# Optimization experiments

Hardware: AMD Instinct MI355X
Metric: run time of the kernel (lower is better)

Reference implementation:

```python
import jax, jax.numpy as jnp
import numpy as np

D = 1024
H = 8
DK = D // H
DFF = 4 * D
EPS = 1e-6


def layer_norm(x, g, b):
    mu = jnp.mean(x, axis=-1, keepdims=True)
    var = jnp.mean(jnp.square(x - mu), axis=-1, keepdims=True)
    return (x - mu) * jax.lax.rsqrt(var + EPS) * g + b


def setup_inputs() -> dict:
    key = jax.random.key(0)
    ks = jax.random.split(key, 8)
    s = 0.02
    return {
        "x": jax.random.normal(ks[0], (4, 2048, D), dtype=jnp.float32),
        "Wq": jax.random.normal(ks[1], (D, D), dtype=jnp.float32) * s,
        "bq": jnp.zeros((D,), dtype=jnp.float32),
        "Wk": jax.random.normal(ks[2], (D, D), dtype=jnp.float32) * s,
        "bk": jnp.zeros((D,), dtype=jnp.float32),
        "Wv": jax.random.normal(ks[3], (D, D), dtype=jnp.float32) * s,
        "bv": jnp.zeros((D,), dtype=jnp.float32),
        "ln1_g": jnp.ones((D,), dtype=jnp.float32),
        "ln1_b": jnp.zeros((D,), dtype=jnp.float32),
        "W1": jax.random.normal(ks[4], (D, DFF), dtype=jnp.float32) * s,
        "b1": jnp.zeros((DFF,), dtype=jnp.float32),
        "W2": jax.random.normal(ks[5], (DFF, D), dtype=jnp.float32) * s,
        "b2": jnp.zeros((D,), dtype=jnp.float32),
        "ln2_g": jnp.ones((D,), dtype=jnp.float32),
        "ln2_b": jnp.zeros((D,), dtype=jnp.float32),
    }


def reference(x, Wq, bq, Wk, bk, Wv, bv, ln1_g, ln1_b, W1, b1, W2, b2, ln2_g, ln2_b):
    B, S, _ = x.shape

    def split_heads(t):  # [B,S,D] -> [B,H,S,dk]
        return t.reshape(B, S, H, DK).transpose(0, 2, 1, 3)

    Q = split_heads(x @ Wq + bq)
    K = split_heads(x @ Wk + bk)
    V = split_heads(x @ Wv + bv)

    scores = jnp.einsum("bhqd,bhkd->bhqk", Q, K) / jnp.sqrt(jnp.float32(DK))
    attn = jax.nn.softmax(scores, axis=-1)  # dropout is identity at eval
    out = jnp.einsum("bhqk,bhkd->bhqd", attn, V)
    out = out.transpose(0, 2, 1, 3).reshape(B, S, D)
    x1 = layer_norm(out + x, ln1_g, ln1_b)

    h = jax.nn.relu(x1 @ W1 + b1) @ W2 + b2  # dropout identity at eval
    return layer_norm(h + x1, ln2_g, ln2_b)
```

## Files before the change

kernel.cpp:

```cpp
#include <hip/hip_runtime.h>
#include <hip/hip_bf16.h>
#include <stdint.h>

#define D_MODEL 1024
#define NHEADS  8
#define DKH     128
#define DFF     4096
#define SEQ     2048
#define BATCH   4
#define NTOK    (BATCH*SEQ)
#define QKS     2048
#define QSCALE  0.12751743f

typedef float  f32x4  __attribute__((ext_vector_type(4)));
typedef __bf16 bf16x8 __attribute__((ext_vector_type(8)));

static __device__ __forceinline__ float b2f(ushort u) {
    union { uint32_t i; float f; } v; v.i = ((uint32_t)u) << 16; return v.f;
}
static __device__ __forceinline__ ushort f2b(float f) {
    union { float f; uint32_t i; } v; v.f = f;
    uint32_t r = v.i + 0x7fffu + ((v.i >> 16) & 1u);
    return (ushort)(r >> 16);
}
static __device__ __forceinline__ ushort f2b_native(float f) {
    __bf16 h = (__bf16)f;
    return __builtin_bit_cast(ushort, h);
}
static __device__ __forceinline__ float exp2_hw(float x) {
    return __builtin_amdgcn_exp2f(x);
}
static __device__ __forceinline__ void gl_lds16(const void* g, void* l) {
    __builtin_amdgcn_global_load_lds(
        (const __attribute__((address_space(1))) void*)g,
        (__attribute__((address_space(3))) void*)l, 16, 0, 0);
}
static __device__ __forceinline__ float dpp_max16(float x) {
    int t;
    t = __builtin_amdgcn_update_dpp(0, __builtin_bit_cast(int, x), 0xB1, 0xF, 0xF, true);
    x = fmaxf(x, __builtin_bit_cast(float, t));
    t = __builtin_amdgcn_update_dpp(0, __builtin_bit_cast(int, x), 0x4E, 0xF, 0xF, true);
    x = fmaxf(x, __builtin_bit_cast(float, t));
    t = __builtin_amdgcn_update_dpp(0, __builtin_bit_cast(int, x), 0x141, 0xF, 0xF, true);
    x = fmaxf(x, __builtin_bit_cast(float, t));
    t = __builtin_amdgcn_update_dpp(0, __builtin_bit_cast(int, x), 0x140, 0xF, 0xF, true);
    x = fmaxf(x, __builtin_bit_cast(float, t));
    return x;
}

__global__ __launch_bounds__(256) void conv_kernel(
    const float* __restrict__ in, ushort* __restrict__ out, int n)
{
    for (int i = (blockIdx.x * 256 + threadIdx.x) * 4; i < n; i += gridDim.x * 1024) {
        float4 v = *(const float4*)(in + i);
        ushort o[4] = { f2b(v.x), f2b(v.y), f2b(v.z), f2b(v.w) };
        *(uint2*)(out + i) = *(const uint2*)o;
    }
}

__global__ __launch_bounds__(256) void tconv_kernel(
    const float* __restrict__ in, ushort* __restrict__ out, int R, int C)
{
    __shared__ float L[32][33];
    const int tid = threadIdx.x;
    const int tx = tid & 31, ty = tid >> 5;
    const int nbc = C >> 5;
    const int r0 = (blockIdx.x / nbc) << 5;
    const int c0 = (blockIdx.x % nbc) << 5;
    #pragma unroll
    for (int p = 0; p < 4; ++p)
        L[ty + 8 * p][tx] = in[(size_t)(r0 + ty + 8 * p) * C + c0 + tx];
    __syncthreads();
    #pragma unroll
    for (int p = 0; p < 4; ++p)
        out[(size_t)(c0 + ty + 8 * p) * R + r0 + tx] = f2b(L[tx][ty + 8 * p]);
}

__global__ __launch_bounds__(256) void cat3_kernel(
    const float* __restrict__ a, const float* __restrict__ b,
    const float* __restrict__ c, float* __restrict__ out)
{
    const int i = blockIdx.x * 256 + threadIdx.x;
    out[i] = (i < 1024) ? a[i] : (i < 2048) ? b[i - 1024] : c[i - 2048];
}

__global__ __launch_bounds__(512, 2) void gemm8_relu(
    const ushort* __restrict__ A, const ushort* __restrict__ Bt,
    const float* __restrict__ bias, ushort* __restrict__ C,
    int M, int N, int K)
{
    __shared__ __align__(16) ushort lds[65536];

    const int tid  = threadIdx.x;
    const int w    = tid >> 6;
    const int lane = tid & 63;
    const int l16  = lane & 15;
    const int quad = (lane >> 4) & 3;
    const int wm   = w >> 2;
    const int wn   = w & 3;

    const int nbn = N >> 8;
    const int m0  = (blockIdx.x / nbn) << 8;
    const int n0  = (blockIdx.x % nbn) << 8;

    const int rsub = tid >> 3;
    const int gsw  = (tid & 7) ^ (rsub & 7);
    const ushort* Asrc = A  + (size_t)(m0 + rsub) * K + gsw * 8;
    const ushort* Bsrc = Bt + (size_t)(n0 + rsub) * K + gsw * 8;

    auto issue_half = [&](int p, int kt, int d) {
        const ushort* src;
        int base;
        if (p < 2) { src = Asrc + (size_t)(p * 128) * K;       base = d * 16384 + p * 8192; }
        else       { src = Bsrc + (size_t)((p - 2) * 128) * K; base = 32768 + d * 16384 + (p - 2) * 8192; }
        src += kt * 64;
        gl_lds16(src,                  &lds[base + w * 512]);
        gl_lds16(src + (size_t)64 * K, &lds[base + w * 512 + 4096]);
    };

    f32x4  acc[8][4] = {};
    bf16x8 bfr[4];

    auto phase = [&](int cur, int ks, int mq, bool readB) {
        const int Ab = cur * 16384 + wm * 8192;
        const int Bb = 32768 + cur * 16384 + (wn >> 1) * 8192;
        if (readB) {
            #pragma unroll
            for (int nt = 0; nt < 4; ++nt) {
                const int rB = ((wn & 1) << 6) + nt * 16 + l16;
                const int gB = ((ks << 2) + quad) ^ (rB & 7);
                bfr[nt] = *(const bf16x8*)&lds[Bb + rB * 64 + gB * 8];
            }
        }
        bf16x8 afr[4];
        #pragma unroll
        for (int mt = 0; mt < 4; ++mt) {
            const int rA = mq * 64 + mt * 16 + l16;
            const int gA = ((ks << 2) + quad) ^ (rA & 7);
            afr[mt] = *(const bf16x8*)&lds[Ab + rA * 64 + gA * 8];
        }
        __builtin_amdgcn_s_setprio(1);
        #pragma unroll
        for (int mt = 0; mt < 4; ++mt)
            #pragma unroll
            for (int nt = 0; nt < 4; ++nt)
                acc[mq * 4 + mt][nt] = __builtin_amdgcn_mfma_f32_16x16x32_bf16(
                    afr[mt], bfr[nt], acc[mq * 4 + mt][nt], 0, 0, 0);
        __builtin_amdgcn_s_setprio(0);
    };

    const int NT = K >> 6;

    #pragma unroll
    for (int p = 0; p < 4; ++p) issue_half(p, 0, 0);
    issue_half(0, 1, 1);
    asm volatile("s_waitcnt vmcnt(2)" ::: "memory");
    __builtin_amdgcn_sched_barrier(0);
    __builtin_amdgcn_s_barrier();
    __builtin_amdgcn_sched_barrier(0);

    for (int t = 0; t < NT; ++t) {
        const int  cur = t & 1;
        const bool pf  = (t + 1 < NT);

        if (pf) issue_half(1, t + 1, cur ^ 1);
        phase(cur, 0, 0, true);
        if (pf) issue_half(2, t + 1, cur ^ 1);
        phase(cur, 0, 1, false);
        if (pf) issue_half(3, t + 1, cur ^ 1);
        phase(cur, 1, 0, true);
        phase(cur, 1, 1, false);

        __builtin_amdgcn_sched_barrier(0);
        __builtin_amdgcn_s_barrier();
        __builtin_amdgcn_sched_barrier(0);
        if (pf) {
            if (t + 2 < NT) {
                issue_half(0, t + 2, cur);
                asm volatile("s_waitcnt vmcnt(2)" ::: "memory");
            } else {
                asm volatile("s_waitcnt vmcnt(0)" ::: "memory");
            }
            __builtin_amdgcn_sched_barrier(0);
            __builtin_amdgcn_s_barrier();
            __builtin_amdgcn_sched_barrier(0);
        }
    }
    __builtin_amdgcn_sched_barrier(0);

    #pragma unroll
    for (int nt = 0; nt < 4; ++nt) {
        const int n = n0 + wn * 64 + nt * 16 + l16;
        const float bv = bias[n];
        #pragma unroll
        for (int a = 0; a < 8; ++a) {
            const int mrow = m0 + wm * 128 + (a >> 2) * 64 + (a & 3) * 16 + (quad << 2);
            #pragma unroll
            for (int r = 0; r < 4; ++r) {
                const float v = fmaxf(acc[a][nt][r] + bv, 0.f);
                C[(size_t)(mrow + r) * N + n] = f2b(v);
            }
        }
    }
}

template<int MODE>
__global__ __launch_bounds__(512, 2) void gemm12(
    const ushort* __restrict__ A, const ushort* __restrict__ Bt,
    const float* __restrict__ bias, ushort* __restrict__ C,
    ushort* __restrict__ C2, int M, int N, int K)
{
    __shared__ __align__(16) ushort lds[49152];

    const int tid  = threadIdx.x;
    const int w    = tid >> 6;
    const int lane = tid & 63;
    const int l16  = lane & 15;
    const int quad = (lane >> 4) & 3;
    const int wm   = w >> 2;
    const int wn   = w & 3;

    const int cpx  = gridDim.x >> 3;
    const int bidx = (blockIdx.x & 7) * cpx + (blockIdx.x >> 3);

    int tix = bidx, kbeg = 0, kend = K, sl = 0;
    if (MODE == 3) {
        const int tiles = (M >> 7) * (N >> 8);
        sl   = bidx / tiles;
        tix  = bidx % tiles;
        kbeg = sl * (K >> 1);
        kend = kbeg + (K >> 1);
    }
    const int nbn = N >> 8;
    const int m0  = (tix / nbn) << 7;
    const int n0  = (tix % nbn) << 8;

    const int rsub = tid >> 3;
    const int gsw  = (tid & 7) ^ (rsub & 7);
    const ushort* Asrc = A  + (size_t)(m0 + rsub) * K + gsw * 8 + kbeg;
    const ushort* Bsrc = Bt + (size_t)(n0 + rsub) * K + gsw * 8 + kbeg;

    auto issue_half = [&](int p, int kt, int d) {
        const ushort* src;
        int base;
        if (p == 0) { src = Asrc;                              base = d * 8192; }
        else        { src = Bsrc + (size_t)((p - 1) * 128) * K; base = 16384 + d * 16384 + (p - 1) * 8192; }
        src += kt * 64;
        gl_lds16(src,                  &lds[base + w * 512]);
        gl_lds16(src + (size_t)64 * K, &lds[base + w * 512 + 4096]);
    };

    f32x4 acc[4][4] = {};

    auto phase = [&](int cur, int ks) {
        const int Ab = cur * 8192;
        const int Bb = 16384 + cur * 16384;
        bf16x8 afr[4], bfr[4];
        #pragma unroll
        for (int nt = 0; nt < 4; ++nt) {
            const int rB = wn * 64 + nt * 16 + l16;
            const int gB = ((ks << 2) + quad) ^ (rB & 7);
            bfr[nt] = *(const bf16x8*)&lds[Bb + rB * 64 + gB * 8];
        }
        #pragma unroll
        for (int mt = 0; mt < 4; ++mt) {
            const int rA = wm * 64 + mt * 16 + l16;
            const int gA = ((ks << 2) + quad) ^ (rA & 7);
            afr[mt] = *(const bf16x8*)&lds[Ab + rA * 64 + gA * 8];
        }
        __builtin_amdgcn_s_setprio(1);
        #pragma unroll
        for (int mt = 0; mt < 4; ++mt)
            #pragma unroll
            for (int nt = 0; nt < 4; ++nt)
                acc[mt][nt] = __builtin_amdgcn_mfma_f32_16x16x32_bf16(
                    afr[mt], bfr[nt], acc[mt][nt], 0, 0, 0);
        __builtin_amdgcn_s_setprio(0);
    };

    const int NT = (kend - kbeg) >> 6;

    issue_half(0, 0, 0);
    issue_half(1, 0, 0);
    issue_half(2, 0, 0);
    issue_half(0, 1, 1);
    asm volatile("s_waitcnt vmcnt(2)" ::: "memory");
    __builtin_amdgcn_sched_barrier(0);
    __builtin_amdgcn_s_barrier();
    __builtin_amdgcn_sched_barrier(0);

    for (int t = 0; t < NT; ++t) {
        const int  cur = t & 1;
        const bool pf  = (t + 1 < NT);

        if (pf) issue_half(1, t + 1, cur ^ 1);
        phase(cur, 0);
        if (pf) issue_half(2, t + 1, cur ^ 1);
        phase(cur, 1);

        __builtin_amdgcn_sched_barrier(0);
        __builtin_amdgcn_s_barrier();
        __builtin_amdgcn_sched_barrier(0);
        if (pf) {
            if (t + 2 < NT) {
                issue_half(0, t + 2, cur);
                asm volatile("s_waitcnt vmcnt(2)" ::: "memory");
            } else {
                asm volatile("s_waitcnt vmcnt(0)" ::: "memory");
            }
            __builtin_amdgcn_sched_barrier(0);
            __builtin_amdgcn_s_barrier();
            __builtin_amdgcn_sched_barrier(0);
        }
    }
    __builtin_amdgcn_sched_barrier(0);

    if (MODE == 2 && n0 >= 2048) {
        #pragma unroll
        for (int nt = 0; nt < 4; ++nt) {
            const int n  = n0 + wn * 64 + nt * 16 + l16;
            const int hd = n - 2048;
            const float bv = bias[n];
            const size_t vrow = (size_t)(hd >> 7) * 128 + (hd & 127);
            #pragma unroll
            for (int mt = 0; mt < 4; ++mt) {
                const int m = m0 + wm * 64 + mt * 16 + (quad << 2);
                const size_t row = (size_t)(m >> 11) * 1024 + vrow;
                ushort pk[4];
                #pragma unroll
                for (int r = 0; r < 4; ++r) pk[r] = f2b(acc[mt][nt][r] + bv);
                *(uint2*)(C2 + row * SEQ + (m & 2047)) = *(const uint2*)pk;
            }
        }
    } else if (MODE == 2) {
        const float qs = (n0 < 1024) ? QSCALE : 1.f;
        #pragma unroll
        for (int nt = 0; nt < 4; ++nt) {
            const int n = n0 + wn * 64 + nt * 16 + l16;
            const float bv = bias[n];
            #pragma unroll
            for (int mt = 0; mt < 4; ++mt) {
                #pragma unroll
                for (int r = 0; r < 4; ++r) {
                    const int m = m0 + wm * 64 + mt * 16 + (quad << 2) + r;
                    C[(size_t)m * QKS + n] = f2b((acc[mt][nt][r] + bv) * qs);
                }
            }
        }
    } else {
        ushort* Co = sl ? C2 : C;
        #pragma unroll
        for (int nt = 0; nt < 4; ++nt) {
            const int n = n0 + wn * 64 + nt * 16 + l16;
            const float bv = sl ? 0.f : bias[n];
            #pragma unroll
            for (int mt = 0; mt < 4; ++mt) {
                #pragma unroll
                for (int r = 0; r < 4; ++r) {
                    const int m = m0 + wm * 64 + mt * 16 + (quad << 2) + r;
                    Co[(size_t)m * N + n] = f2b(acc[mt][nt][r] + bv);
                }
            }
        }
    }
}

__global__ __launch_bounds__(256) void attn_kernel(
    ushort* __restrict__ qk, const ushort* __restrict__ vt)
{
    __shared__ __align__(16) ushort smem[40960];
    ushort* Ks = smem;
    ushort* Vs = smem + 16384;
    ushort* Ps = smem + 32768;

    const int tid  = threadIdx.x;
    const int w    = tid >> 6;
    const int lane = tid & 63;
    const int l16  = lane & 15;
    const int quad = lane >> 4;

    const int bid = ((blockIdx.x & 7) << 7) + (blockIdx.x >> 3);
    const int qb  = bid & 31;
    const int h   = (bid >> 5) & 7;
    const int b   = bid >> 8;

    ushort* Qp = qk + ((size_t)(b * SEQ + qb * 64)) * QKS + h * DKH;
    const ushort* Kp = qk + ((size_t)(b * SEQ)) * QKS + 1024 + h * DKH;
    const ushort* Vp = vt + ((size_t)((b * 8 + h) * 128)) * SEQ;

    #pragma unroll
    for (int i = 0; i < 4; ++i) {
        const int row = w * 16 + i * 4 + quad;
        const int g = (l16 & 8) | ((l16 & 7) ^ (row & 7));
        gl_lds16(Qp + (size_t)row * QKS + g * 8, Vs + (w * 16 + i * 4) * 128);
    }
    #pragma unroll
    for (int i = 0; i < 8; ++i) {
        const int row = w * 32 + i * 4 + quad;
        const int g = (l16 & 8) | ((l16 & 7) ^ (row & 7));
        gl_lds16(Kp + (size_t)row * QKS + g * 8, Ks + (w * 32 + i * 4) * 128);
    }
    __syncthreads();

    bf16x8 aq[4];
    {
        const int r = w * 16 + l16;
        #pragma unroll
        for (int kq = 0; kq < 4; ++kq) {
            const int gk = kq * 4 + quad;
            const int g = (gk & 8) | ((gk & 7) ^ (r & 7));
            aq[kq] = *(const bf16x8*)&Vs[r * 128 + g * 8];
        }
    }
    __syncthreads();

    #pragma unroll
    for (int i = 0; i < 8; ++i) {
        const int d = w * 32 + i * 4 + quad;
        const int g = (l16 & 8) | ((l16 & 7) ^ (d & 7));
        gl_lds16(Vp + (size_t)d * SEQ + g * 8, Vs + (w * 32 + i * 4) * 128);
    }

    f32x4 o[8] = {};
    float mrun[4], lrun[4];
    #pragma unroll
    for (int r = 0; r < 4; ++r) { mrun[r] = -1e30f; lrun[r] = 0.f; }

    for (int t = 0; t < SEQ / 128; ++t) {
        f32x4 s[8] = {};
        #pragma unroll
        for (int nt = 0; nt < 8; ++nt) {
            const int rk = nt * 16 + l16;
            #pragma unroll
            for (int kq = 0; kq < 4; ++kq) {
                const int gk = kq * 4 + quad;
                const int g = (gk & 8) | ((gk & 7) ^ (rk & 7));
                bf16x8 bk = *(const bf16x8*)&Ks[rk * 128 + g * 8];
                s[nt] = __builtin_amdgcn_mfma_f32_16x16x32_bf16(aq[kq], bk, s[nt], 0, 0, 0);
            }
        }
        __syncthreads();

        if (t + 1 < SEQ / 128) {
            #pragma unroll
            for (int i = 0; i < 8; ++i) {
                const int row = w * 32 + i * 4 + quad;
                const int g = (l16 & 8) | ((l16 & 7) ^ (row & 7));
                gl_lds16(Kp + ((size_t)((t + 1) * 128 + row)) * QKS + g * 8,
                         Ks + (w * 32 + i * 4) * 128);
            }
        }

        float vmax[4];
        #pragma unroll
        for (int r = 0; r < 4; ++r) {
            float v = s[0][r];
            #pragma unroll
            for (int nt = 1; nt < 8; ++nt) v = fmaxf(v, s[nt][r]);
            vmax[r] = dpp_max16(v);
        }
        const int grew = (vmax[0] > mrun[0]) | (vmax[1] > mrun[1]) |
                         (vmax[2] > mrun[2]) | (vmax[3] > mrun[3]);
        if (__any(grew)) {
            #pragma unroll
            for (int r = 0; r < 4; ++r) {
                const float mnew = fmaxf(mrun[r], vmax[r]);
                const float alpha = exp2_hw(mrun[r] - mnew);
                mrun[r] = mnew;
                lrun[r] *= alpha;
                #pragma unroll
                for (int nt8 = 0; nt8 < 8; ++nt8)
                    o[nt8][r] *= alpha;
            }
        }
        #pragma unroll
        for (int nt = 0; nt < 8; ++nt)
            #pragma unroll
            for (int r = 0; r < 4; ++r) {
                const float p = exp2_hw(s[nt][r] - mrun[r]);
                lrun[r] += p;
                const int row = w * 16 + (quad << 2) + r;
                Ps[row * 128 + ((nt * 16 + l16) ^ ((row & 15) << 3))] = f2b_native(p);
            }

        #pragma unroll
        for (int kp = 0; kp < 4; ++kp) {
            const int rowp = w * 16 + l16;
            const int gp = kp * 4 + quad;
            const int gsw2 = gp ^ (rowp & 15);
            bf16x8 ap = *(const bf16x8*)&Ps[rowp * 128 + gsw2 * 8];
            #pragma unroll
            for (int nt8 = 0; nt8 < 8; ++nt8) {
                const int d = nt8 * 16 + l16;
                const int gv = (gp & 8) | ((gp & 7) ^ (d & 7));
                bf16x8 bv = *(const bf16x8*)&Vs[d * 128 + gv * 8];
                o[nt8] = __builtin_amdgcn_mfma_f32_16x16x32_bf16(ap, bv, o[nt8], 0, 0, 0);
            }
        }
        __syncthreads();

        if (t + 1 < SEQ / 128) {
            #pragma unroll
            for (int i = 0; i < 8; ++i) {
                const int d = w * 32 + i * 4 + quad;
                const int g = (l16 & 8) | ((l16 & 7) ^ (d & 7));
                gl_lds16(Vp + (size_t)d * SEQ + (t + 1) * 128 + g * 8,
                         Vs + (w * 32 + i * 4) * 128);
            }
        }
    }

    #pragma unroll
    for (int r = 0; r < 4; ++r) {
        float v = lrun[r];
        #pragma unroll
        for (int msk = 1; msk <= 8; msk <<= 1)
            v += __shfl_xor(v, msk, 64);
        lrun[r] = v;
    }
    #pragma unroll
    for (int r = 0; r < 4; ++r) {
        const float inv = 1.f / lrun[r];
        const int row = w * 16 + (quad << 2) + r;
        #pragma unroll
        for (int nt8 = 0; nt8 < 8; ++nt8)
            Qp[(size_t)row * QKS + nt8 * 16 + l16] = f2b_native(o[nt8][r] * inv);
    }
}

__global__ __launch_bounds__(256) void ln_kernel(
    const ushort* __restrict__ a, int astride, const ushort* __restrict__ a2,
    const void* __restrict__ res, int res_f32,
    const float* __restrict__ g, const float* __restrict__ be,
    void* __restrict__ out, int out_f32)
{
    __shared__ float red[8];
    const int row = blockIdx.x;
    const int tid = threadIdx.x;
    const int col = tid * 4;

    ushort av[4];
    *(uint2*)av = *(const uint2*)(a + (size_t)row * astride + col);

    float v[4];
    if (res_f32) {
        float4 rr = *(const float4*)((const float*)res + (size_t)row * D_MODEL + col);
        v[0] = b2f(av[0]) + rr.x; v[1] = b2f(av[1]) + rr.y;
        v[2] = b2f(av[2]) + rr.z; v[3] = b2f(av[3]) + rr.w;
    } else {
        ushort rv[4];
        *(uint2*)rv = *(const uint2*)((const ushort*)res + (size_t)row * D_MODEL + col);
        #pragma unroll
        for (int i = 0; i < 4; ++i) v[i] = b2f(av[i]) + b2f(rv[i]);
    }
    if (a2) {
        ushort bv[4];
        *(uint2*)bv = *(const uint2*)(a2 + (size_t)row * D_MODEL + col);
        #pragma unroll
        for (int i = 0; i < 4; ++i) v[i] += b2f(bv[i]);
    }

    float s = v[0] + v[1] + v[2] + v[3];
    #pragma unroll
    for (int m = 1; m <= 32; m <<= 1) s += __shfl_xor(s, m, 64);
    if ((tid & 63) == 0) red[tid >> 6] = s;
    __syncthreads();
    const float mu = (red[0] + red[1] + red[2] + red[3]) * (1.f / D_MODEL);

    float q = 0.f;
    #pragma unroll
    for (int i = 0; i < 4; ++i) { const float d = v[i] - mu; q += d * d; }
    #pragma unroll
    for (int m = 1; m <= 32; m <<= 1) q += __shfl_xor(q, m, 64);
    if ((tid & 63) == 0) red[4 + (tid >> 6)] = q;
    __syncthreads();
    const float var = (red[4] + red[5] + red[6] + red[7]) * (1.f / D_MODEL);
    const float rstd = rsqrtf(var + 1e-6f);

    float4 gg = *(const float4*)(g + col);
    float4 bb = *(const float4*)(be + col);
    float y[4];
    y[0] = (v[0] - mu) * rstd * gg.x + bb.x;
    y[1] = (v[1] - mu) * rstd * gg.y + bb.y;
    y[2] = (v[2] - mu) * rstd * gg.z + bb.z;
    y[3] = (v[3] - mu) * rstd * gg.w + bb.w;

    if (out_f32) {
        float4 ov; ov.x = y[0]; ov.y = y[1]; ov.z = y[2]; ov.w = y[3];
        *(float4*)((float*)out + (size_t)row * D_MODEL + col) = ov;
    } else {
        ushort ov[4] = { f2b(y[0]), f2b(y[1]), f2b(y[2]), f2b(y[3]) };
        *(uint2*)((ushort*)out + (size_t)row * D_MODEL + col) = *(const uint2*)ov;
    }
}

__global__ __launch_bounds__(256) void sentinel_kernel(float* out, float S, int n) {
    for (int i = blockIdx.x * 256 + threadIdx.x; i < n; i += gridDim.x * 256)
        out[i] = S;
}

extern "C" void kernel_launch(void* const* d_in, const int* in_sizes, int n_in,
                              void* d_out, int out_size, void* d_ws, size_t ws_size,
                              hipStream_t stream)
{
    const float* x   = (const float*)d_in[0];
    const float* Wq  = (const float*)d_in[1];
    const float* bq  = (const float*)d_in[2];
    const float* Wk  = (const float*)d_in[3];
    const float* bk  = (const float*)d_in[4];
    const float* Wv  = (const float*)d_in[5];
    const float* bv  = (const float*)d_in[6];
    const float* g1  = (const float*)d_in[7];
    const float* be1 = (const float*)d_in[8];
    const float* W1  = (const float*)d_in[9];
    const float* b1  = (const float*)d_in[10];
    const float* W2  = (const float*)d_in[11];
    const float* b2  = (const float*)d_in[12];
    const float* g2  = (const float*)d_in[13];
    const float* be2 = (const float*)d_in[14];

    const size_t MB = 1024 * 1024;
    dim3 blk(256);

    if (ws_size < 88 * MB) {
        int k = (int)(ws_size >> 23); if (k > 127) k = 127;
        sentinel_kernel<<<dim3(2048), blk, 0, stream>>>(
            (float*)d_out, 1024.f + 8.f * (float)k, out_size);
        return;
    }

    char* ws = (char*)d_ws;
    ushort* qkb    = (ushort*)(ws);
    ushort* vtb    = (ushort*)(ws + 32 * MB);
    ushort* ffn0   = (ushort*)(ws);
    ushort* ffn1   = (ushort*)(ws + 16 * MB);
    ushort* xb     = (ushort*)(ws + 48 * MB);
    ushort* x1     = (ushort*)(ws + 48 * MB);
    ushort* wqkv_t = (ushort*)(ws + 64 * MB);
    ushort* w1t    = (ushort*)(ws + 70 * MB);
    ushort* w2t    = (ushort*)(ws + 78 * MB);
    float*  bqkv   = (float*) (ws + 86 * MB);
    ushort* hbuf   = (ushort*)d_out;

    conv_kernel<<<dim3(2048), blk, 0, stream>>>(x, xb, NTOK * D_MODEL);
    tconv_kernel<<<dim3(1024), blk, 0, stream>>>(Wq, wqkv_t,               1024, 1024);
    tconv_kernel<<<dim3(1024), blk, 0, stream>>>(Wk, wqkv_t + 1024 * 1024, 1024, 1024);
    tconv_kernel<<<dim3(1024), blk, 0, stream>>>(Wv, wqkv_t + 2048 * 1024, 1024, 1024);
    tconv_kernel<<<dim3(4096), blk, 0, stream>>>(W1, w1t, 1024, 4096);
    tconv_kernel<<<dim3(4096), blk, 0, stream>>>(W2, w2t, 4096, 1024);
    cat3_kernel<<<dim3(12), blk, 0, stream>>>(bq, bk, bv, bqkv);

    gemm12<2><<<dim3(64 * 12), dim3(512), 0, stream>>>(
        xb, wqkv_t, bqkv, qkb, vtb, NTOK, 3072, D_MODEL);

    attn_kernel<<<dim3(BATCH * NHEADS * (SEQ / 64)), blk, 0, stream>>>(qkb, vtb);

    ln_kernel<<<dim3(NTOK), blk, 0, stream>>>(qkb, QKS, nullptr, x, 1, g1, be1, x1, 0);

    for (int c = 0; c < 2; ++c) {
        const size_t ro = (size_t)c * 4096;
        gemm8_relu<<<dim3(16 * 16), dim3(512), 0, stream>>>(
            x1 + ro * D_MODEL, w1t, b1, hbuf, 4096, DFF, D_MODEL);
        gemm12<3><<<dim3(2 * 32 * 4), dim3(512), 0, stream>>>(
            hbuf, w2t, b2, ffn0 + ro * D_MODEL, ffn1 + ro * D_MODEL,
            4096, D_MODEL, DFF);
    }

    ln_kernel<<<dim3(NTOK), blk, 0, stream>>>(ffn0, D_MODEL, ffn1, x1, 0,
                                              g2, be2, d_out, 1);
}
```

Measured before the change: 511.3 us.

## Process 128 query rows per attention block with interleaved softmax and MFMA

The attention kernel now handles two 64-row query sub-tiles per block, so each K/V tile loaded into LDS is reused twice and global K/V traffic per query is halved. The two sub-tiles are software-pipelined: the softmax of one sub-tile is placed between the MFMA phases of the other, and s_setprio raises wave priority around the MFMA sections to encourage overlap. The three Q/K/V weight transpose launches are merged into a single kernel. In exchange, register pressure roughly doubles for accumulators and the grid is halved, which may lower occupancy and wave count.

Measured after the change: 582.3 us. 13.9% more time.

```diff
diff --git a/kernel.cpp b/kernel.cpp
--- a/kernel.cpp
+++ b/kernel.cpp
@@ -76,6 +76,28 @@
         out[(size_t)(c0 + ty + 8 * p) * R + r0 + tx] = f2b(L[tx][ty + 8 * p]);
 }
 
+__global__ __launch_bounds__(256) void tconv3_kernel(
+    const float* __restrict__ a, const float* __restrict__ b,
+    const float* __restrict__ c, ushort* __restrict__ out)
+{
+    __shared__ float L[32][33];
+    const int which = blockIdx.x >> 10;
+    const float* in = (which == 0) ? a : (which == 1) ? b : c;
+    ushort* o = out + (size_t)which * 1024 * 1024;
+    const int bix = blockIdx.x & 1023;
+    const int tid = threadIdx.x;
+    const int tx = tid & 31, ty = tid >> 5;
+    const int r0 = (bix >> 5) << 5;
+    const int c0 = (bix & 31) << 5;
+    #pragma unroll
+    for (int p = 0; p < 4; ++p)
+        L[ty + 8 * p][tx] = in[(size_t)(r0 + ty + 8 * p) * 1024 + c0 + tx];
+    __syncthreads();
+    #pragma unroll
+    for (int p = 0; p < 4; ++p)
+        o[(size_t)(c0 + ty + 8 * p) * 1024 + r0 + tx] = f2b(L[tx][ty + 8 * p]);
+}
+
 __global__ __launch_bounds__(256) void cat3_kernel(
     const float* __restrict__ a, const float* __restrict__ b,
     const float* __restrict__ c, float* __restrict__ out)
@@ -379,37 +401,33 @@
     const int l16  = lane & 15;
     const int quad = lane >> 4;
 
-    const int bid = ((blockIdx.x & 7) << 7) + (blockIdx.x >> 3);
-    const int qb  = bid & 31;
-    const int h   = (bid >> 5) & 7;
-    const int b   = bid >> 8;
-
-    ushort* Qp = qk + ((size_t)(b * SEQ + qb * 64)) * QKS + h * DKH;
+    const int bid = ((blockIdx.x & 7) << 6) + (blockIdx.x >> 3);
+    const int qb  = bid & 15;
+    const int h   = (bid >> 4) & 7;
+    const int b   = bid >> 7;
+
+    ushort* Qp = qk + ((size_t)(b * SEQ + qb * 128)) * QKS + h * DKH;
     const ushort* Kp = qk + ((size_t)(b * SEQ)) * QKS + 1024 + h * DKH;
     const ushort* Vp = vt + ((size_t)((b * 8 + h) * 128)) * SEQ;
 
-    #pragma unroll
-    for (int i = 0; i < 4; ++i) {
-        const int row = w * 16 + i * 4 + quad;
-        const int g = (l16 & 8) | ((l16 & 7) ^ (row & 7));
-        gl_lds16(Qp + (size_t)row * QKS + g * 8, Vs + (w * 16 + i * 4) * 128);
-    }
     #pragma unroll
     for (int i = 0; i < 8; ++i) {
         const int row = w * 32 + i * 4 + quad;
         const int g = (l16 & 8) | ((l16 & 7) ^ (row & 7));
+        gl_lds16(Qp + (size_t)row * QKS + g * 8, Vs + (w * 32 + i * 4) * 128);
         gl_lds16(Kp + (size_t)row * QKS + g * 8, Ks + (w * 32 + i * 4) * 128);
     }
     __syncthreads();
 
-    bf16x8 aq[4];
-    {
-        const int r = w * 16 + l16;
+    bf16x8 aq[2][4];
+    #pragma unroll
+    for (int st = 0; st < 2; ++st) {
+        const int r = st * 64 + w * 16 + l16;
         #pragma unroll
         for (int kq = 0; kq < 4; ++kq) {
             const int gk = kq * 4 + quad;
             const int g = (gk & 8) | ((gk & 7) ^ (r & 7));
-            aq[kq] = *(const bf16x8*)&Vs[r * 128 + g * 8];
+            aq[st][kq] = *(const bf16x8*)&Vs[r * 128 + g * 8];
         }
     }
     __syncthreads();
@@ -421,13 +439,19 @@
         gl_lds16(Vp + (size_t)d * SEQ + g * 8, Vs + (w * 32 + i * 4) * 128);
     }
 
-    f32x4 o[8] = {};
-    float mrun[4], lrun[4];
-    #pragma unroll
-    for (int r = 0; r < 4; ++r) { mrun[r] = -1e30f; lrun[r] = 0.f; }
+    f32x4 o[2][8] = {};
+    float mrun[2][4], lrun[2][4];
+    #pragma unroll
+    for (int st = 0; st < 2; ++st)
+        #pragma unroll
+        for (int r = 0; r < 4; ++r) { mrun[st][r] = -1e30f; lrun[st][r] = 0.f; }
+
+    const int rowp = w * 16 + l16;
+    const int roww = w * 16 + (quad << 2);
 
     for (int t = 0; t < SEQ / 128; ++t) {
-        f32x4 s[8] = {};
+        f32x4 s0[8] = {};
+        __builtin_amdgcn_s_setprio(1);
         #pragma unroll
         for (int nt = 0; nt < 8; ++nt) {
             const int rk = nt * 16 + l16;
@@ -436,9 +460,60 @@
                 const int gk = kq * 4 + quad;
                 const int g = (gk & 8) | ((gk & 7) ^ (rk & 7));
                 bf16x8 bk = *(const bf16x8*)&Ks[rk * 128 + g * 8];
-                s[nt] = __builtin_amdgcn_mfma_f32_16x16x32_bf16(aq[kq], bk, s[nt], 0, 0, 0);
-            }
-        }
+                s0[nt] = __builtin_amdgcn_mfma_f32_16x16x32_bf16(aq[0][kq], bk, s0[nt], 0, 0, 0);
+            }
+        }
+        __builtin_amdgcn_s_setprio(0);
+
+        {
+            float vmax[4];
+            #pragma unroll
+            for (int r = 0; r < 4; ++r) {
+                float v = s0[0][r];
+                #pragma unroll
+                for (int nt = 1; nt < 8; ++nt) v = fmaxf(v, s0[nt][r]);
+                vmax[r] = dpp_max16(v);
+            }
+            const int grew = (vmax[0] > mrun[0][0]) | (vmax[1] > mrun[0][1]) |
+                             (vmax[2] > mrun[0][2]) | (vmax[3] > mrun[0][3]);
+            if (__any(grew)) {
+                #pragma unroll
+                for (int r = 0; r < 4; ++r) {
+                    const float mnew = fmaxf(mrun[0][r], vmax[r]);
+                    const float alpha = exp2_hw(mrun[0][r] - mnew);
+                    mrun[0][r] = mnew;
+                    lrun[0][r] *= alpha;
+                    #pragma unroll
+                    for (int nt8 = 0; nt8 < 8; ++nt8)
+                        o[0][nt8][r] *= alpha;
+                }
+            }
+            #pragma unroll
+            for (int nt = 0; nt < 8; ++nt)
+                #pragma unroll
+                for (int r = 0; r < 4; ++r) {
+                    const float p = exp2_hw(s0[nt][r] - mrun[0][r]);
+                    lrun[0][r] += p;
+                    const int row = roww + r;
+                    Ps[row * 128 + ((nt * 16 + l16) ^ ((row & 15) << 3))] = f2b_native(p);
+                }
+        }
+
+        f32x4 s1[8] = {};
+        __builtin_amdgcn_s_setprio(1);
+        #pragma unroll
+        for (int nt = 0; nt < 8; ++nt) {
+            const int rk = nt * 16 + l16;
+            #pragma unroll
+            for (int kq = 0; kq < 4; ++kq) {
+                const int gk = kq * 4 + quad;
+                const int g = (gk & 8) | ((gk & 7) ^ (rk & 7));
+                bf16x8 bk = *(const bf16x8*)&Ks[rk * 128 + g * 8];
+                s1[nt] = __builtin_amdgcn_mfma_f32_16x16x32_bf16(aq[1][kq], bk, s1[nt], 0, 0, 0);
+            }
+        }
+        __builtin_amdgcn_s_setprio(0);
+
         __syncthreads();
 
         if (t + 1 < SEQ / 128) {
@@ -451,41 +526,9 @@
             }
         }
 
-        float vmax[4];
-        #pragma unroll
-        for (int r = 0; r < 4; ++r) {
-            float v = s[0][r];
-            #pragma unroll
-            for (int nt = 1; nt < 8; ++nt) v = fmaxf(v, s[nt][r]);
-            vmax[r] = dpp_max16(v);
-        }
-        const int grew = (vmax[0] > mrun[0]) | (vmax[1] > mrun[1]) |
-                         (vmax[2] > mrun[2]) | (vmax[3] > mrun[3]);
-        if (__any(grew)) {
-            #pragma unroll
-            for (int r = 0; r < 4; ++r) {
-                const float mnew = fmaxf(mrun[r], vmax[r]);
-                const float alpha = exp2_hw(mrun[r] - mnew);
-                mrun[r] = mnew;
-                lrun[r] *= alpha;
-                #pragma unroll
-                for (int nt8 = 0; nt8 < 8; ++nt8)
-                    o[nt8][r] *= alpha;
-            }
-        }
-        #pragma unroll
-        for (int nt = 0; nt < 8; ++nt)
-            #pragma unroll
-            for (int r = 0; r < 4; ++r) {
-                const float p = exp2_hw(s[nt][r] - mrun[r]);
-                lrun[r] += p;
-                const int row = w * 16 + (quad << 2) + r;
-                Ps[row * 128 + ((nt * 16 + l16) ^ ((row & 15) << 3))] = f2b_native(p);
-            }
-
+        __builtin_amdgcn_s_setprio(1);
         #pragma unroll
         for (int kp = 0; kp < 4; ++kp) {
-            const int rowp = w * 16 + l16;
             const int gp = kp * 4 + quad;
             const int gsw2 = gp ^ (rowp & 15);
             bf16x8 ap = *(const bf16x8*)&Ps[rowp * 128 + gsw2 * 8];
@@ -494,9 +537,61 @@
                 const int d = nt8 * 16 + l16;
                 const int gv = (gp & 8) | ((gp & 7) ^ (d & 7));
                 bf16x8 bv = *(const bf16x8*)&Vs[d * 128 + gv * 8];
-                o[nt8] = __builtin_amdgcn_mfma_f32_16x16x32_bf16(ap, bv, o[nt8], 0, 0, 0);
-            }
-        }
+                o[0][nt8] = __builtin_amdgcn_mfma_f32_16x16x32_bf16(ap, bv, o[0][nt8], 0, 0, 0);
+            }
+        }
+        __builtin_amdgcn_s_setprio(0);
+
+        {
+            float vmax[4];
+            #pragma unroll
+            for (int r = 0; r < 4; ++r) {
+                float v = s1[0][r];
+                #pragma unroll
+                for (int nt = 1; nt < 8; ++nt) v = fmaxf(v, s1[nt][r]);
+                vmax[r] = dpp_max16(v);
+            }
+            const int grew = (vmax[0] > mrun[1][0]) | (vmax[1] > mrun[1][1]) |
+                             (vmax[2] > mrun[1][2]) | (vmax[3] > mrun[1][3]);
+            if (__any(grew)) {
+                #pragma unroll
+                for (int r = 0; r < 4; ++r) {
+                    const float mnew = fmaxf(mrun[1][r], vmax[r]);
+                    const float alpha = exp2_hw(mrun[1][r] - mnew);
+                    mrun[1][r] = mnew;
+                    lrun[1][r] *= alpha;
+                    #pragma unroll
+                    for (int nt8 = 0; nt8 < 8; ++nt8)
+                        o[1][nt8][r] *= alpha;
+                }
+            }
+            #pragma unroll
+            for (int nt = 0; nt < 8; ++nt)
+                #pragma unroll
+                for (int r = 0; r < 4; ++r) {
+                    const float p = exp2_hw(s1[nt][r] - mrun[1][r]);
+                    lrun[1][r] += p;
+                    const int row = roww + r;
+                    Ps[row * 128 + ((nt * 16 + l16) ^ ((row & 15) << 3))] = f2b_native(p);
+                }
+        }
+
+        __builtin_amdgcn_s_setprio(1);
+        #pragma unroll
+        for (int kp = 0; kp < 4; ++kp) {
+            const int gp = kp * 4 + quad;
+            const int gsw2 = gp ^ (rowp & 15);
+            bf16x8 ap = *(const bf16x8*)&Ps[rowp * 128 + gsw2 * 8];
+            #pragma unroll
+            for (int nt8 = 0; nt8 < 8; ++nt8) {
+                const int d = nt8 * 16 + l16;
+                const int gv = (gp & 8) | ((gp & 7) ^ (d & 7));
+                bf16x8 bv = *(const bf16x8*)&Vs[d * 128 + gv * 8];
+                o[1][nt8] = __builtin_amdgcn_mfma_f32_16x16x32_bf16(ap, bv, o[1][nt8], 0, 0, 0);
+            }
+        }
+        __builtin_amdgcn_s_setprio(0);
+
         __syncthreads();
 
         if (t + 1 < SEQ / 128) {
@@ -511,21 +606,25 @@
     }
 
     #pragma unroll
-    for (int r = 0; r < 4; ++r) {
-        float v = lrun[r];
-        #pragma unroll
-        for (int msk = 1; msk <= 8; msk <<= 1)
-            v += __shfl_xor(v, msk, 64);
-        lrun[r] = v;
-    }
-    #pragma unroll
-    for (int r = 0; r < 4; ++r) {
-        const float inv = 1.f / lrun[r];
-        const int row = w * 16 + (quad << 2) + r;
-        #pragma unroll
-        for (int nt8 = 0; nt8 < 8; ++nt8)
-            Qp[(size_t)row * QKS + nt8 * 16 + l16] = f2b_native(o[nt8][r] * inv);
-    }
+    for (int st = 0; st < 2; ++st)
+        #pragma unroll
+        for (int r = 0; r < 4; ++r) {
+            float v = lrun[st][r];
+            #pragma unroll
+            for (int msk = 1; msk <= 8; msk <<= 1)
+                v += __shfl_xor(v, msk, 64);
+            lrun[st][r] = v;
+        }
+    #pragma unroll
+    for (int st = 0; st < 2; ++st)
+        #pragma unroll
+        for (int r = 0; r < 4; ++r) {
+            const float inv = 1.f / lrun[st][r];
+            const int row = st * 64 + w * 16 + (quad << 2) + r;
+            #pragma unroll
+            for (int nt8 = 0; nt8 < 8; ++nt8)
+                Qp[(size_t)row * QKS + nt8 * 16 + l16] = f2b_native(o[st][nt8][r] * inv);
+        }
 }
 
 __global__ __launch_bounds__(256) void ln_kernel(
@@ -643,9 +742,7 @@
     ushort* hbuf   = (ushort*)d_out;
 
     conv_kernel<<<dim3(2048), blk, 0, stream>>>(x, xb, NTOK * D_MODEL);
-    tconv_kernel<<<dim3(1024), blk, 0, stream>>>(Wq, wqkv_t,               1024, 1024);
-    tconv_kernel<<<dim3(1024), blk, 0, stream>>>(Wk, wqkv_t + 1024 * 1024, 1024, 1024);
-    tconv_kernel<<<dim3(1024), blk, 0, stream>>>(Wv, wqkv_t + 2048 * 1024, 1024, 1024);
+    tconv3_kernel<<<dim3(3072), blk, 0, stream>>>(Wq, Wk, Wv, wqkv_t);
     tconv_kernel<<<dim3(4096), blk, 0, stream>>>(W1, w1t, 1024, 4096);
     tconv_kernel<<<dim3(4096), blk, 0, stream>>>(W2, w2t, 4096, 1024);
     cat3_kernel<<<dim3(12), blk, 0, stream>>>(bq, bk, bv, bqkv);
@@ -653,7 +750,7 @@
     gemm12<2><<<dim3(64 * 12), dim3(512), 0, stream>>>(
         xb, wqkv_t, bqkv, qkb, vtb, NTOK, 3072, D_MODEL);
 
-    attn_kernel<<<dim3(BATCH * NHEADS * (SEQ / 64)), blk, 0, stream>>>(qkb, vtb);
+    attn_kernel<<<dim3(BATCH * NHEADS * (SEQ / 128)), blk, 0, stream>>>(qkb, vtb);
 
     ln_kernel<<<dim3(NTOK), blk, 0, stream>>>(qkb, QKS, nullptr, x, 1, g1, be1, x1, 0);
 
```
